# Optimization experiments

Measured on AMD Instinct MI355X. Metric: run time of the kernel, lower is better.

The kernel has to match this reference:

```python
import jax, jax.numpy as jnp
import numpy as np
import math

LENS = 64  # sliding window length (init arg `lens`)

def setup_inputs() -> dict:
    key = jax.random.key(0)
    k1, k2 = jax.random.split(key)
    N, D = 4096, 512
    X = jax.random.normal(k1, (N, D), dtype=jnp.float32)
    # nn.Linear(d, d, bias=False) weight, applied as x @ W.T
    W = jax.random.normal(k2, (D, D), dtype=jnp.float32) * (1.0 / math.sqrt(D))
    return {"X": X, "W": W}

def reference(X, W):
    N, d = X.shape
    B = N - LENS  # number of sliding windows
    # sliding-window gather: h_his[b] = X[b : b+LENS]
    idx = jnp.arange(B)[:, None] + jnp.arange(LENS)[None, :]  # [B, LENS]
    h_his = X[idx]            # [B, LENS, d]
    h_cur = X[LENS:]          # [B, d]  (index_cur = lens..N-1)
    # attention: score = bmm(linear(kv), q[..., None]) / sqrt(d)
    kv_proj = jnp.einsum('bld,ed->ble', h_his, W)            # [B, LENS, d]
    score = jnp.einsum('ble,be->bl', kv_proj, h_cur)[..., None] / math.sqrt(d)  # [B, LENS, 1]
    # faithful to original: softmax over last (size-1) axis -> all ones
    alpha = jax.nn.softmax(score, axis=-1)                   # [B, LENS, 1]
    attn_out = jnp.einsum('bl,bld->bd', alpha[..., 0], h_his)  # [B, d]
    # dropout(0.3) is eval-mode identity
    H = jnp.concatenate([X[:LENS], attn_out], axis=0) + X    # [N, d]
    h_cur_full = jnp.concatenate([X[:LENS], h_cur], axis=0)  # [N, d]
    return jnp.concatenate([H, h_cur_full], axis=-1)         # [N, 2d]
```

## Files before the change

kernel.cpp:

```cpp
#include <hip/hip_runtime.h>


#define LENS 64
#define RT 8
#define C4 128

__global__ __launch_bounds__(256) void chunk8_kernel(const float4* __restrict__ X4,
                                                     float4* __restrict__ C8,
                                                     int nChunks) {
    const int t  = blockIdx.x * 256 + threadIdx.x;
    const int c4 = t & (C4 - 1);
    const int k  = t >> 7;
    if (k >= nChunks) return;
    const float4* p = X4 + (size_t)k * 8 * C4 + c4;
    float4 s = make_float4(0.f, 0.f, 0.f, 0.f);
#pragma unroll
    for (int j = 0; j < 8; ++j) {
        float4 x = p[(size_t)j * C4];
        s.x += x.x; s.y += x.y; s.z += x.z; s.w += x.w;
    }
    C8[(size_t)k * C4 + c4] = s;
}

__global__ __launch_bounds__(256) void winsum_kernel(const float4* __restrict__ X4,
                                                     const float4* __restrict__ C8,
                                                     float4* __restrict__ O4,
                                                     int N) {
    const int c4   = threadIdx.x & (C4 - 1);
    const int half = threadIdx.x >> 7;
    const int i0   = blockIdx.x * (2 * RT) + half * RT;
    if (i0 >= N) return;

    if (i0 < LENS) {
#pragma unroll
        for (int k = 0; k < RT; ++k) {
            const int i = i0 + k;
            float4 x = X4[(size_t)i * C4 + c4];
            float4 h = make_float4(2.f * x.x, 2.f * x.y, 2.f * x.z, 2.f * x.w);
            O4[(size_t)i * (2 * C4) + c4]      = h;
            O4[(size_t)i * (2 * C4) + C4 + c4] = x;
        }
        return;
    }

    const int m = i0 >> 3;
    float4 w = make_float4(0.f, 0.f, 0.f, 0.f);
#pragma unroll
    for (int q = 0; q < 8; ++q) {
        float4 cs = C8[(size_t)(m - 8 + q) * C4 + c4];
        w.x += cs.x; w.y += cs.y; w.z += cs.z; w.w += cs.w;
    }

    float4 hist[RT - 1];
    const float4* ph = X4 + (size_t)(i0 - LENS) * C4 + c4;
#pragma unroll
    for (int j = 0; j < RT - 1; ++j) hist[j] = ph[(size_t)j * C4];

#pragma unroll
    for (int k = 0; k < RT; ++k) {
        const int i = i0 + k;
        float4 x = X4[(size_t)i * C4 + c4];
        float4 h = make_float4(x.x + w.x, x.y + w.y, x.z + w.z, x.w + w.w);
        O4[(size_t)i * (2 * C4) + c4]      = h;
        O4[(size_t)i * (2 * C4) + C4 + c4] = x;
        if (k < RT - 1) {
            float4 old = hist[k];
            w.x += x.x - old.x;
            w.y += x.y - old.y;
            w.z += x.z - old.z;
            w.w += x.w - old.w;
        }
    }
}

extern "C" void kernel_launch(void* const* d_in, const int* in_sizes, int n_in,
                              void* d_out, int out_size, void* d_ws, size_t ws_size,
                              hipStream_t stream) {
    const float* X = (const float*)d_in[0];
    float* O = (float*)d_out;
    float* C = (float*)d_ws;

    const int D = 512;
    const int N = in_sizes[0] / D;
    const int nChunks = N / 8;

    chunk8_kernel<<<(nChunks * C4 + 255) / 256, 256, 0, stream>>>(
        (const float4*)X, (float4*)C, nChunks);

    const int rows_per_block = 2 * RT;
    winsum_kernel<<<(N + rows_per_block - 1) / rows_per_block, 256, 0, stream>>>(
        (const float4*)X, (const float4*)C, (float4*)O, N);
}
```

Before: 69.20 us.

## Fuse chunk-sum and window-sum kernels into one LDS-tiled kernel

```diff
diff --git a/kernel.cpp b/kernel.cpp
--- a/kernel.cpp
+++ b/kernel.cpp
@@ -2,69 +2,75 @@
 
 
 #define LENS 64
-#define RT 8
-#define C4 128
+#define C4   128
+#define CS   16
+#define NT   128
 
-__global__ __launch_bounds__(256) void chunk8_kernel(const float4* __restrict__ X4,
-                                                     float4* __restrict__ C8,
-                                                     int nChunks) {
-    const int t  = blockIdx.x * 256 + threadIdx.x;
-    const int c4 = t & (C4 - 1);
-    const int k  = t >> 7;
-    if (k >= nChunks) return;
-    const float4* p = X4 + (size_t)k * 8 * C4 + c4;
-    float4 s = make_float4(0.f, 0.f, 0.f, 0.f);
+__global__ __launch_bounds__(NT) void fused_win_kernel(const float4* __restrict__ X4,
+                                                       float4* __restrict__ O4) {
+    __shared__ float4 raw[128][CS];
+    __shared__ float4 chk[16][CS];
+
+    const int g   = blockIdx.x;
+    const int c4b = blockIdx.y * CS;
+    const int tid = threadIdx.x;
+    const int c   = tid & (CS - 1);
+
+    if (g == 0) {
+        const int q = tid >> 4;
 #pragma unroll
-    for (int j = 0; j < 8; ++j) {
-        float4 x = p[(size_t)j * C4];
-        s.x += x.x; s.y += x.y; s.z += x.z; s.w += x.w;
-    }
-    C8[(size_t)k * C4 + c4] = s;
-}
-
-__global__ __launch_bounds__(256) void winsum_kernel(const float4* __restrict__ X4,
-                                                     const float4* __restrict__ C8,
-                                                     float4* __restrict__ O4,
-                                                     int N) {
-    const int c4   = threadIdx.x & (C4 - 1);
-    const int half = threadIdx.x >> 7;
-    const int i0   = blockIdx.x * (2 * RT) + half * RT;
-    if (i0 >= N) return;
-
-    if (i0 < LENS) {
-#pragma unroll
-        for (int k = 0; k < RT; ++k) {
-            const int i = i0 + k;
-            float4 x = X4[(size_t)i * C4 + c4];
-            float4 h = make_float4(2.f * x.x, 2.f * x.y, 2.f * x.z, 2.f * x.w);
-            O4[(size_t)i * (2 * C4) + c4]      = h;
-            O4[(size_t)i * (2 * C4) + C4 + c4] = x;
+        for (int k = 0; k < 8; ++k) {
+            const int i = q * 8 + k;
+            const float4 x = X4[(size_t)i * C4 + c4b + c];
+            O4[(size_t)i * (2 * C4) + c4b + c] =
+                make_float4(2.f * x.x, 2.f * x.y, 2.f * x.z, 2.f * x.w);
+            O4[(size_t)i * (2 * C4) + C4 + c4b + c] = x;
         }
         return;
     }
 
-    const int m = i0 >> 3;
+    const int R0 = g * 64 - LENS;
+
+    {
+        const int k = tid >> 4;
+#pragma unroll
+        for (int kk = 0; kk < 2; ++kk) {
+            const int ch = k + kk * 8;
+            const float4* gp = X4 + (size_t)(R0 + ch * 8) * C4 + c4b + c;
+            float4 s = make_float4(0.f, 0.f, 0.f, 0.f);
+#pragma unroll
+            for (int j = 0; j < 8; ++j) {
+                const float4 x = gp[(size_t)j * C4];
+                raw[ch * 8 + j][c] = x;
+                s.x += x.x; s.y += x.y; s.z += x.z; s.w += x.w;
+            }
+            chk[ch][c] = s;
+        }
+    }
+    __syncthreads();
+
+    const int q  = tid >> 4;
+    const int i0 = g * 64 + q * 8;
+
     float4 w = make_float4(0.f, 0.f, 0.f, 0.f);
 #pragma unroll
-    for (int q = 0; q < 8; ++q) {
-        float4 cs = C8[(size_t)(m - 8 + q) * C4 + c4];
+    for (int r = 0; r < 8; ++r) {
+        const float4 cs = chk[q + r][c];
         w.x += cs.x; w.y += cs.y; w.z += cs.z; w.w += cs.w;
     }
 
-    float4 hist[RT - 1];
-    const float4* ph = X4 + (size_t)(i0 - LENS) * C4 + c4;
+    float4 hist[7];
 #pragma unroll
-    for (int j = 0; j < RT - 1; ++j) hist[j] = ph[(size_t)j * C4];
+    for (int j = 0; j < 7; ++j) hist[j] = raw[q * 8 + j][c];
 
 #pragma unroll
-    for (int k = 0; k < RT; ++k) {
-        const int i = i0 + k;
-        float4 x = X4[(size_t)i * C4 + c4];
-        float4 h = make_float4(x.x + w.x, x.y + w.y, x.z + w.z, x.w + w.w);
-        O4[(size_t)i * (2 * C4) + c4]      = h;
-        O4[(size_t)i * (2 * C4) + C4 + c4] = x;
-        if (k < RT - 1) {
-            float4 old = hist[k];
+    for (int k = 0; k < 8; ++k) {
+        const float4 x = raw[64 + q * 8 + k][c];
+        O4[(size_t)(i0 + k) * (2 * C4) + c4b + c] =
+            make_float4(x.x + w.x, x.y + w.y, x.z + w.z, x.w + w.w);
+        O4[(size_t)(i0 + k) * (2 * C4) + C4 + c4b + c] = x;
+        if (k < 7) {
+            const float4 old = hist[k];
             w.x += x.x - old.x;
             w.y += x.y - old.y;
             w.z += x.z - old.z;
@@ -78,16 +84,10 @@
                               hipStream_t stream) {
     const float* X = (const float*)d_in[0];
     float* O = (float*)d_out;
-    float* C = (float*)d_ws;
 
     const int D = 512;
     const int N = in_sizes[0] / D;
-    const int nChunks = N / 8;
 
-    chunk8_kernel<<<(nChunks * C4 + 255) / 256, 256, 0, stream>>>(
-        (const float4*)X, (float4*)C, nChunks);
-
-    const int rows_per_block = 2 * RT;
-    winsum_kernel<<<(N + rows_per_block - 1) / rows_per_block, 256, 0, stream>>>(
-        (const float4*)X, (const float4*)C, (float4*)O, N);
+    dim3 grid(N / 64, C4 / CS);
+    fused_win_kernel<<<grid, NT, 0, stream>>>((const float4*)X, (float4*)O);
 }
```

Result: faster. 67.22 us (-2.9%).
